# Performance work log

Hardware: AMD Instinct MI355X
Metric: run time of the kernel (lower is better)

Reference implementation:

```python
import jax, jax.numpy as jnp
import numpy as np

NEG_SLOPE = 0.2

def setup_inputs() -> dict:
    key = jax.random.key(0)
    k1, k2, k3, k4 = jax.random.split(key, 4)
    N, K, C_IN, C_OUT = 8192, 4, 512, 512
    inputs = jax.random.normal(k1, (N, C_IN), dtype=jnp.float32)
    adj_set = jax.random.uniform(k2, (K, N, N), dtype=jnp.float32)
    att = jax.random.uniform(k3, (K,), dtype=jnp.float32)
    # xavier_uniform for w
    limit = float(np.sqrt(6.0 / (C_IN + C_OUT)))
    w = jax.random.uniform(k4, (C_IN, C_OUT), minval=-limit, maxval=limit, dtype=jnp.float32)
    b = jnp.zeros((C_OUT,), dtype=jnp.float32)
    return {"inputs": inputs, "adj_set": adj_set, "att": att, "w": w, "b": b}

def reference(inputs, adj_set, att, w, b):
    # support: [N, C_out]
    support = inputs @ w + b
    # residual=True path: outputs = sum_i att[i] * (adj_i @ support)
    #                             = (sum_i att[i] * adj_i) @ support
    combined_adj = jnp.einsum('k,knm->nm', att, adj_set)  # [N, N]
    outputs = combined_adj @ support                       # [N, C_out]
    # LeakyReLU(negative_slope=0.2)
    return jnp.where(outputs >= 0, outputs, NEG_SLOPE * outputs)
```

## Files before the change

### kernel.cpp

```cpp
#include <hip/hip_runtime.h>

#define LP  40
#define LPB 72

typedef __attribute__((ext_vector_type(8))) short short8;
typedef __attribute__((ext_vector_type(4))) short short4t;
typedef __attribute__((ext_vector_type(4))) float f32x4;

__device__ __forceinline__ short f2bf(float f) {
  unsigned u = __builtin_bit_cast(unsigned, f);
  u += 0x7FFFu + ((u >> 16) & 1u);
  return (short)(u >> 16);
}

__device__ __forceinline__ float lrelu(float v) { return v >= 0.f ? v : 0.2f * v; }

__global__ __launch_bounds__(256) void k_wt(const float* __restrict__ w,
                                            short* __restrict__ wt) {
  __shared__ float t[64][65];
  int c0 = (blockIdx.x & 7) * 64;
  int n0 = (blockIdx.x >> 3) * 64;
  int r  = threadIdx.x >> 4;
  int q4 = (threadIdx.x & 15) * 4;
  for (int i = 0; i < 4; i++) {
    int c = r + i * 16;
    f32x4 v = *(const f32x4*)(w + (size_t)(c0 + c) * 512 + (n0 + q4));
    t[c][q4 + 0] = v[0]; t[c][q4 + 1] = v[1]; t[c][q4 + 2] = v[2]; t[c][q4 + 3] = v[3];
  }
  __syncthreads();
  for (int i = 0; i < 4; i++) {
    int n = r + i * 16;
    short4t o;
    for (int j = 0; j < 4; j++) o[j] = f2bf(t[q4 + j][n]);
    *(short4t*)(wt + (size_t)(n0 + n) * 512 + (c0 + q4)) = o;
  }
}

__global__ __launch_bounds__(512, 2) void k_support(const float* __restrict__ inp,
                                                    const short* __restrict__ wt,
                                                    const float* __restrict__ bias,
                                                    short* __restrict__ sup) {
  __shared__ __align__(16) short As[512 * LP];
  __shared__ __align__(16) short Bs[64 * LP];
  const int tid = threadIdx.x;
  const int m0 = blockIdx.x * 64;
  const int wave = tid >> 6, lane = tid & 63;
  const int wn = wave >> 1, wm = wave & 1;
  const int lr = lane & 15, lk = lane >> 4;
  const int bm = tid >> 3, bk = (tid & 7) * 4;
  f32x4 acc[8][2] = {};
  short8 ar[4]; f32x4 br;
  auto loadA = [&](int s) {
    const short* p = wt + (size_t)tid * 512 + s * 32;
    ar[0] = *(const short8*)(p);      ar[1] = *(const short8*)(p + 8);
    ar[2] = *(const short8*)(p + 16); ar[3] = *(const short8*)(p + 24);
  };
  auto loadB = [&](int s) {
    br = *(const f32x4*)(inp + (size_t)(m0 + bm) * 512 + s * 32 + bk);
  };
  loadA(0); loadB(0);
  for (int s = 0; s < 16; s++) {
    short* ad = As + tid * LP;
    *(short8*)(ad) = ar[0]; *(short8*)(ad + 8) = ar[1];
    *(short8*)(ad + 16) = ar[2]; *(short8*)(ad + 24) = ar[3];
    short4t bo;
    for (int j = 0; j < 4; j++) bo[j] = f2bf(br[j]);
    *(short4t*)(Bs + bm * LP + bk) = bo;
    __syncthreads();
    if (s + 1 < 16) { loadA(s + 1); loadB(s + 1); }
    short8 af[8], bfr[2];
    for (int nf = 0; nf < 8; nf++)
      af[nf] = *(const short8*)(As + (wn * 128 + nf * 16 + lr) * LP + lk * 8);
    for (int mf = 0; mf < 2; mf++)
      bfr[mf] = *(const short8*)(Bs + (wm * 32 + mf * 16 + lr) * LP + lk * 8);
    for (int nf = 0; nf < 8; nf++)
      for (int mf = 0; mf < 2; mf++)
        acc[nf][mf] = __builtin_amdgcn_mfma_f32_16x16x32_bf16(af[nf], bfr[mf], acc[nf][mf], 0, 0, 0);
    __syncthreads();
  }
  for (int nf = 0; nf < 8; nf++) {
    int nb = wn * 128 + nf * 16 + lk * 4;
    for (int mf = 0; mf < 2; mf++) {
      int m = m0 + wm * 32 + mf * 16 + lr;
      for (int j = 0; j < 4; j++) {
        int n = nb + j;
        sup[(size_t)n * 8192 + m] = f2bf(acc[nf][mf][j] + bias[n]);
      }
    }
  }
}

#define ISSUEA(SL, S) {                                                         \
    const float* p_ = abase + (size_t)(S) * 64;                                 \
    R[SL][0] = __builtin_nontemporal_load((const f32x4*)(p_));                  \
    R[SL][1] = __builtin_nontemporal_load((const f32x4*)(p_ + 4));              \
    R[SL][2] = __builtin_nontemporal_load((const f32x4*)(p_ + (1ull << 26)));   \
    R[SL][3] = __builtin_nontemporal_load((const f32x4*)(p_ + (1ull << 26) + 4));\
    R[SL][4] = __builtin_nontemporal_load((const f32x4*)(p_ + (2ull << 26)));   \
    R[SL][5] = __builtin_nontemporal_load((const f32x4*)(p_ + (2ull << 26) + 4));\
    R[SL][6] = __builtin_nontemporal_load((const f32x4*)(p_ + (3ull << 26)));   \
    R[SL][7] = __builtin_nontemporal_load((const f32x4*)(p_ + (3ull << 26) + 4));\
  }

#define ISSUEF(SL, S) {                                                         \
    const short* q_ = supp + (size_t)(S) * 64;                                  \
    AF[SL][0][0] = *(const short8*)(q_);                                        \
    AF[SL][0][1] = *(const short8*)(q_ + 32);                                   \
    AF[SL][1][0] = *(const short8*)(q_ + (size_t)16 * 8192);                    \
    AF[SL][1][1] = *(const short8*)(q_ + (size_t)16 * 8192 + 32);               \
    AF[SL][2][0] = *(const short8*)(q_ + (size_t)32 * 8192);                    \
    AF[SL][2][1] = *(const short8*)(q_ + (size_t)32 * 8192 + 32);               \
    AF[SL][3][0] = *(const short8*)(q_ + (size_t)48 * 8192);                    \
    AF[SL][3][1] = *(const short8*)(q_ + (size_t)48 * 8192 + 32);               \
  }

#define STEPK(U) {                                                              \
    const int s_ = s0 + (U);                                                    \
    ISSUEF(((U) + 1) & 1, (s_ + 1) & (NSTEPS - 1))                              \
    __builtin_amdgcn_sched_barrier(0);                                          \
    asm volatile("s_waitcnt vmcnt(16)" ::: "memory");                           \
    __builtin_amdgcn_sched_barrier(0);                                          \
    f32x4 cA_, cB_;                                                             \
    _Pragma("unroll") for (int e = 0; e < 4; e++) {                             \
      cA_[e] = t0 * R[(U)][0][e] + t1 * R[(U)][2][e]                            \
             + t2 * R[(U)][4][e] + t3 * R[(U)][6][e];                           \
      cB_[e] = t0 * R[(U)][1][e] + t1 * R[(U)][3][e]                            \
             + t2 * R[(U)][5][e] + t3 * R[(U)][7][e];                           \
    }                                                                           \
    short8 o_;                                                                  \
    _Pragma("unroll") for (int e = 0; e < 4; e++) {                             \
      o_[e] = f2bf(cA_[e]); o_[4 + e] = f2bf(cB_[e]);                           \
    }                                                                           \
    *(short8*)(Bs[(U)] + r * LPB + q * 8) = o_;                                 \
    ISSUEA((U), (s_ + 2) & (NSTEPS - 1))                                        \
    __builtin_amdgcn_sched_barrier(0);                                          \
    asm volatile("s_waitcnt lgkmcnt(0)" ::: "memory");                          \
    __builtin_amdgcn_sched_barrier(0);                                          \
    __builtin_amdgcn_s_barrier();                                               \
    __builtin_amdgcn_sched_barrier(0);                                          \
    _Pragma("unroll") for (int h = 0; h < 2; h++) {                             \
      _Pragma("unroll") for (int mf = 0; mf < 4; mf++) {                        \
        short8 bfr = *(const short8*)(Bs[(U)] + (mf * 16 + lr) * LPB + h * 32 + lk * 8); \
        _Pragma("unroll") for (int nf = 0; nf < 4; nf++)                        \
          acc[nf][mf] = __builtin_amdgcn_mfma_f32_16x16x32_bf16(                \
              AF[(U)][nf][h], bfr, acc[nf][mf], 0, 0, 0);                       \
      }                                                                         \
    }                                                                           \
  }

template <int KSPLIT>
__global__ __launch_bounds__(512, 2) void k_main(const float* __restrict__ adj,
                                                 const float* __restrict__ att,
                                                 const short* __restrict__ sup,
                                                 float* __restrict__ part,
                                                 float* __restrict__ outp) {
  constexpr int NSTEPS = 8192 / KSPLIT / 64;
  __shared__ __align__(16) short Bs[2][64 * LPB];
  const int tid = threadIdx.x;
  const int b = blockIdx.x;
  const int xpk = 8 / KSPLIT;
  const int xcd = b & 7;
  const int kc = xcd / xpk;
  const int m0 = ((b >> 3) * xpk + (xcd % xpk)) * 64;
  const int kbase = kc * (8192 / KSPLIT);
  const float t0 = att[0], t1 = att[1], t2 = att[2], t3 = att[3];
  const int wave = tid >> 6, lane = tid & 63;
  const int lr = lane & 15, lk = lane >> 4;
  const int r = tid >> 3, q = tid & 7;
  f32x4 acc[4][4] = {};
  const float* abase = adj + (size_t)(m0 + r) * 8192 + kbase + q * 8;
  const short* supp = sup + (size_t)(wave * 64 + lr) * 8192 + kbase + lk * 8;
  f32x4 R[2][8];
  short8 AF[2][4][2];

  ISSUEA(0, 0) ISSUEF(0, 0) ISSUEA(1, 1)
  for (int s0 = 0; s0 < NSTEPS; s0 += 2) {
    STEPK(0) STEPK(1)
  }

#pragma unroll
  for (int nf = 0; nf < 4; nf++) {
    int n = wave * 64 + nf * 16 + lk * 4;
#pragma unroll
    for (int mf = 0; mf < 4; mf++) {
      int m = m0 + mf * 16 + lr;
      f32x4 v = acc[nf][mf];
      if (KSPLIT == 1) {
        for (int j = 0; j < 4; j++) v[j] = lrelu(v[j]);
        __builtin_nontemporal_store(v, (f32x4*)(outp + (size_t)m * 512 + n));
      } else {
        __builtin_nontemporal_store(v, (f32x4*)(part + ((size_t)kc << 22) + (size_t)m * 512 + n));
      }
    }
  }
}

__global__ __launch_bounds__(256) void k_reduce(const float* __restrict__ part,
                                                float* __restrict__ outp, int ksplit) {
  const size_t total = (size_t)8192 * 512 / 4;
  for (size_t i = (size_t)blockIdx.x * 256 + threadIdx.x; i < total;
       i += (size_t)gridDim.x * 256) {
    f32x4 a = __builtin_nontemporal_load((const f32x4*)(part + i * 4));
    for (int k = 1; k < ksplit; k++) {
      f32x4 bv = __builtin_nontemporal_load((const f32x4*)(part + ((size_t)k << 22) + i * 4));
      for (int j = 0; j < 4; j++) a[j] += bv[j];
    }
    f32x4 v;
    for (int j = 0; j < 4; j++) v[j] = lrelu(a[j]);
    __builtin_nontemporal_store(v, (f32x4*)(outp + i * 4));
  }
}

extern "C" void kernel_launch(void* const* d_in, const int* in_sizes, int n_in,
                              void* d_out, int out_size, void* d_ws, size_t ws_size,
                              hipStream_t stream) {
  const float* inputs = (const float*)d_in[0];
  const float* adj    = (const float*)d_in[1];
  const float* att    = (const float*)d_in[2];
  const float* w      = (const float*)d_in[3];
  const float* bias   = (const float*)d_in[4];
  float* outp = (float*)d_out;

  char* ws = (char*)d_ws;
  short* sup  = (short*)(ws);
  short* wt   = (short*)(ws + (8u << 20));
  float* part = (float*)(ws + (9u << 20));

  const size_t base = (9ull << 20), psz = (1ull << 24);

  k_wt<<<64, 256, 0, stream>>>(w, wt);
  k_support<<<128, 512, 0, stream>>>(inputs, wt, bias, sup);

  if (ws_size >= base + 2 * psz) {
    k_main<2><<<256, 512, 0, stream>>>(adj, att, sup, part, outp);
    k_reduce<<<1024, 256, 0, stream>>>(part, outp, 2);
  } else {
    k_main<1><<<128, 512, 0, stream>>>(adj, att, sup, part, outp);
  }
}
```

Before: 336.9 us.

## Restructure main GEMM to 256-thread blocks, 32-wide K steps, and 4-way K split

```diff
diff --git a/kernel.cpp b/kernel.cpp
--- a/kernel.cpp
+++ b/kernel.cpp
@@ -1,7 +1,7 @@
 #include <hip/hip_runtime.h>
 
 #define LP  40
-#define LPB 72
+#define LPB 40
 
 typedef __attribute__((ext_vector_type(8))) short short8;
 typedef __attribute__((ext_vector_type(4))) short short4t;
@@ -91,7 +91,7 @@
 }
 
 #define ISSUEA(SL, S) {                                                         \
-    const float* p_ = abase + (size_t)(S) * 64;                                 \
+    const float* p_ = abase + (size_t)(S) * 32;                                 \
     R[SL][0] = __builtin_nontemporal_load((const f32x4*)(p_));                  \
     R[SL][1] = __builtin_nontemporal_load((const f32x4*)(p_ + 4));              \
     R[SL][2] = __builtin_nontemporal_load((const f32x4*)(p_ + (1ull << 26)));   \
@@ -102,23 +102,11 @@
     R[SL][7] = __builtin_nontemporal_load((const f32x4*)(p_ + (3ull << 26) + 4));\
   }
 
-#define ISSUEF(SL, S) {                                                         \
-    const short* q_ = supp + (size_t)(S) * 64;                                  \
-    AF[SL][0][0] = *(const short8*)(q_);                                        \
-    AF[SL][0][1] = *(const short8*)(q_ + 32);                                   \
-    AF[SL][1][0] = *(const short8*)(q_ + (size_t)16 * 8192);                    \
-    AF[SL][1][1] = *(const short8*)(q_ + (size_t)16 * 8192 + 32);               \
-    AF[SL][2][0] = *(const short8*)(q_ + (size_t)32 * 8192);                    \
-    AF[SL][2][1] = *(const short8*)(q_ + (size_t)32 * 8192 + 32);               \
-    AF[SL][3][0] = *(const short8*)(q_ + (size_t)48 * 8192);                    \
-    AF[SL][3][1] = *(const short8*)(q_ + (size_t)48 * 8192 + 32);               \
-  }
-
 #define STEPK(U) {                                                              \
     const int s_ = s0 + (U);                                                    \
-    ISSUEF(((U) + 1) & 1, (s_ + 1) & (NSTEPS - 1))                              \
-    __builtin_amdgcn_sched_barrier(0);                                          \
-    asm volatile("s_waitcnt vmcnt(16)" ::: "memory");                           \
+    _Pragma("unroll") for (int nf = 0; nf < 8; nf++)                            \
+      AF[nf] = *(const short8*)(supp + (size_t)(nf * 16) * 8192 + (size_t)s_ * 32); \
+    ISSUEA((U) ^ 1, (s_ + 1) & (NSTEPS - 1))                                    \
     __builtin_amdgcn_sched_barrier(0);                                          \
     f32x4 cA_, cB_;                                                             \
     _Pragma("unroll") for (int e = 0; e < 4; e++) {                             \
@@ -132,29 +120,26 @@
       o_[e] = f2bf(cA_[e]); o_[4 + e] = f2bf(cB_[e]);                           \
     }                                                                           \
     *(short8*)(Bs[(U)] + r * LPB + q * 8) = o_;                                 \
-    ISSUEA((U), (s_ + 2) & (NSTEPS - 1))                                        \
     __builtin_amdgcn_sched_barrier(0);                                          \
     asm volatile("s_waitcnt lgkmcnt(0)" ::: "memory");                          \
     __builtin_amdgcn_sched_barrier(0);                                          \
     __builtin_amdgcn_s_barrier();                                               \
     __builtin_amdgcn_sched_barrier(0);                                          \
-    _Pragma("unroll") for (int h = 0; h < 2; h++) {                             \
-      _Pragma("unroll") for (int mf = 0; mf < 4; mf++) {                        \
-        short8 bfr = *(const short8*)(Bs[(U)] + (mf * 16 + lr) * LPB + h * 32 + lk * 8); \
-        _Pragma("unroll") for (int nf = 0; nf < 4; nf++)                        \
-          acc[nf][mf] = __builtin_amdgcn_mfma_f32_16x16x32_bf16(                \
-              AF[(U)][nf][h], bfr, acc[nf][mf], 0, 0, 0);                       \
-      }                                                                         \
+    _Pragma("unroll") for (int mf = 0; mf < 4; mf++) {                          \
+      short8 bfr = *(const short8*)(Bs[(U)] + (mf * 16 + lr) * LPB + lk * 8);   \
+      _Pragma("unroll") for (int nf = 0; nf < 8; nf++)                          \
+        acc[nf][mf] = __builtin_amdgcn_mfma_f32_16x16x32_bf16(AF[nf], bfr,      \
+                                                              acc[nf][mf], 0, 0, 0); \
     }                                                                           \
   }
 
 template <int KSPLIT>
-__global__ __launch_bounds__(512, 2) void k_main(const float* __restrict__ adj,
+__global__ __launch_bounds__(256, 2) void k_main(const float* __restrict__ adj,
                                                  const float* __restrict__ att,
                                                  const short* __restrict__ sup,
                                                  float* __restrict__ part,
                                                  float* __restrict__ outp) {
-  constexpr int NSTEPS = 8192 / KSPLIT / 64;
+  constexpr int NSTEPS = 8192 / KSPLIT / 32;
   __shared__ __align__(16) short Bs[2][64 * LPB];
   const int tid = threadIdx.x;
   const int b = blockIdx.x;
@@ -166,21 +151,21 @@
   const float t0 = att[0], t1 = att[1], t2 = att[2], t3 = att[3];
   const int wave = tid >> 6, lane = tid & 63;
   const int lr = lane & 15, lk = lane >> 4;
-  const int r = tid >> 3, q = tid & 7;
-  f32x4 acc[4][4] = {};
+  const int r = tid >> 2, q = tid & 3;
+  f32x4 acc[8][4] = {};
   const float* abase = adj + (size_t)(m0 + r) * 8192 + kbase + q * 8;
-  const short* supp = sup + (size_t)(wave * 64 + lr) * 8192 + kbase + lk * 8;
+  const short* supp = sup + (size_t)(wave * 128 + lr) * 8192 + kbase + lk * 8;
   f32x4 R[2][8];
-  short8 AF[2][4][2];
-
-  ISSUEA(0, 0) ISSUEF(0, 0) ISSUEA(1, 1)
+  short8 AF[8];
+
+  ISSUEA(0, 0)
   for (int s0 = 0; s0 < NSTEPS; s0 += 2) {
     STEPK(0) STEPK(1)
   }
 
 #pragma unroll
-  for (int nf = 0; nf < 4; nf++) {
-    int n = wave * 64 + nf * 16 + lk * 4;
+  for (int nf = 0; nf < 8; nf++) {
+    int n = wave * 128 + nf * 16 + lk * 4;
 #pragma unroll
     for (int mf = 0; mf < 4; mf++) {
       int m = m0 + mf * 16 + lr;
@@ -231,10 +216,13 @@
   k_wt<<<64, 256, 0, stream>>>(w, wt);
   k_support<<<128, 512, 0, stream>>>(inputs, wt, bias, sup);
 
-  if (ws_size >= base + 2 * psz) {
-    k_main<2><<<256, 512, 0, stream>>>(adj, att, sup, part, outp);
+  if (ws_size >= base + 4 * psz) {
+    k_main<4><<<512, 256, 0, stream>>>(adj, att, sup, part, outp);
+    k_reduce<<<1024, 256, 0, stream>>>(part, outp, 4);
+  } else if (ws_size >= base + 2 * psz) {
+    k_main<2><<<256, 256, 0, stream>>>(adj, att, sup, part, outp);
     k_reduce<<<1024, 256, 0, stream>>>(part, outp, 2);
   } else {
-    k_main<1><<<128, 512, 0, stream>>>(adj, att, sup, part, outp);
-  }
-}
+    k_main<1><<<128, 256, 0, stream>>>(adj, att, sup, part, outp);
+  }
+}
```

After: 406.7 us. +20.7%, slower.
